# Performance work log

Measured on AMD Instinct MI355X. Metric: run time of the kernel, lower is better.

## Reference

```python
import jax, jax.numpy as jnp
import numpy as np

DIM = 512
HEADS = 8
DHEAD = 64
WIN = 128
QK_SCALE = 8.0
LN_EPS = 1e-5


def setup_inputs() -> dict:
    key = jax.random.key(0)
    ks = jax.random.split(key, 5)
    B, N = 8, 4096
    x = jax.random.normal(ks[0], (B, N, DIM), jnp.float32)
    w_qkv = jax.random.normal(ks[1], (3 * HEADS * DHEAD, DIM), jnp.float32) * 0.02
    w_out = jax.random.normal(ks[2], (DIM, HEADS * DHEAD), jnp.float32) * 0.02
    b_out = jnp.zeros((DIM,), jnp.float32)
    w_ff1 = jax.random.normal(ks[3], (4 * DIM, DIM), jnp.float32) * 0.02
    w_ff2 = jax.random.normal(ks[4], (DIM, 4 * DIM), jnp.float32) * 0.02
    return {
        'x': x, 'w_qkv': w_qkv,
        'q_scale': jnp.ones((DHEAD,), jnp.float32),
        'k_scale': jnp.ones((DHEAD,), jnp.float32),
        'w_out': w_out, 'b_out': b_out,
        'ln1_g': jnp.ones((DIM,), jnp.float32), 'ln1_b': jnp.zeros((DIM,), jnp.float32),
        'ff_ln_g': jnp.ones((DIM,), jnp.float32), 'ff_ln_b': jnp.zeros((DIM,), jnp.float32),
        'w_ff1': w_ff1, 'w_ff2': w_ff2,
    }


def _ln(x, g, b):
    m = jnp.mean(x, axis=-1, keepdims=True)
    v = jnp.mean((x - m) ** 2, axis=-1, keepdims=True)
    return (x - m) * jax.lax.rsqrt(v + LN_EPS) * g + b


def _l2norm(t):
    return t / jnp.clip(jnp.linalg.norm(t, axis=-1, keepdims=True), 1e-12)


def _rotary(t, pos):
    # t: (B, H, N, DHEAD); standard (non-xpos) rotary, half-split style
    inv_freq = 1.0 / (10000.0 ** (jnp.arange(0, DHEAD, 2, dtype=jnp.float32) / DHEAD))
    freqs = pos[:, None] * inv_freq                      # (N, DHEAD/2)
    emb = jnp.concatenate([freqs, freqs], axis=-1)       # (N, DHEAD)
    cos, sin = jnp.cos(emb), jnp.sin(emb)
    t1, t2 = t[..., : DHEAD // 2], t[..., DHEAD // 2:]
    rot = jnp.concatenate([-t2, t1], axis=-1)
    return t * cos + rot * sin


def reference(x, w_qkv, q_scale, k_scale, w_out, b_out, ln1_g, ln1_b,
              ff_ln_g, ff_ln_b, w_ff1, w_ff2):
    B, N, D = x.shape
    nw = N // WIN

    # ---- LocalMHA (prenorm, qk-rmsnorm, sliding window, causal) ----
    h = _ln(x, ln1_g, ln1_b)
    qkv = h @ w_qkv.T                                    # (B, N, 3*H*DHEAD)
    q, k, v = jnp.split(qkv, 3, axis=-1)

    def to_heads(t):
        return t.reshape(B, N, HEADS, DHEAD).transpose(0, 2, 1, 3)  # (B,H,N,d)

    q, k, v = to_heads(q), to_heads(k), to_heads(v)
    q = _l2norm(q) * q_scale
    k = _l2norm(k) * k_scale
    pos = jnp.arange(N, dtype=jnp.float32)
    q = _rotary(q, pos)
    k = _rotary(k, pos)

    # bucket into windows; keys/values look back one window
    bq = q.reshape(B, HEADS, nw, WIN, DHEAD)
    bk = k.reshape(B, HEADS, nw, WIN, DHEAD)
    bv = v.reshape(B, HEADS, nw, WIN, DHEAD)

    def look_back(t):
        prev = jnp.concatenate([jnp.zeros_like(t[:, :, :1]), t[:, :, :-1]], axis=2)
        return jnp.concatenate([prev, t], axis=3)

    kk, vv = look_back(bk), look_back(bv)

    qpos = jnp.arange(N, dtype=jnp.int32).reshape(nw, WIN)
    kprev = jnp.concatenate([jnp.full((1, WIN), -1, jnp.int32), qpos[:-1]], axis=0)
    kpos = jnp.concatenate([kprev, qpos], axis=1)
    mask = (qpos[:, :, None] >= kpos[:, None, :]) & (kpos[:, None, :] >= 0)

    sim = jnp.einsum('bhnid,bhnjd->bhnij', bq, kk) * QK_SCALE
    sim = jnp.where(mask, sim, -1e9)
    attn = jax.nn.softmax(sim, axis=-1)
    out = jnp.einsum('bhnij,bhnjd->bhnid', attn, vv)
    out = out.reshape(B, HEADS, N, DHEAD).transpose(0, 2, 1, 3).reshape(B, N, HEADS * DHEAD)
    x = x + out @ w_out.T + b_out

    # ---- FeedForward: LN -> Linear(4D, no bias) -> GELU -> Linear(D, no bias) ----
    hf = _ln(x, ff_ln_g, ff_ln_b)
    ff = jax.nn.gelu(hf @ w_ff1.T, approximate=False) @ w_ff2.T
    return x + ff
```

## Files before the change

### kernel.cpp

```cpp
#include <hip/hip_runtime.h>
#include <cstdint>
#include <cstddef>

typedef __bf16 bf16;
typedef __bf16 bf16x8 __attribute__((ext_vector_type(8)));
typedef float f32x4 __attribute__((ext_vector_type(4)));

#define DEV static __device__ __forceinline__

constexpr int BATCH = 8;
constexpr int SEQ = 4096;
constexpr int DIM = 512;
constexpr int HEADS = 8;
constexpr int DH = 64;
constexpr int WIN = 128;
constexpr int NW = SEQ / WIN;
constexpr int TOK = BATCH * SEQ;
constexpr float EPS = 1e-5f;

constexpr size_t R_EL   = (size_t)TOK * DIM;
constexpr size_t C_QKV  = 0;
constexpr size_t C_WOUT = 786432;
constexpr size_t C_WF1  = 1048576;
constexpr size_t C_WF2  = 2097152;
constexpr size_t C_SM   = 3145728;
constexpr size_t P_EL   = 3148416;

DEV void gload_lds16(const void* g, void* l) {
  __builtin_amdgcn_global_load_lds((__attribute__((address_space(1))) void*)g,
                                   (__attribute__((address_space(3))) void*)l,
                                   16, 0, 0);
}

DEV f32x4 mfma16(bf16x8 a, bf16x8 b, f32x4 c) {
  return __builtin_amdgcn_mfma_f32_16x16x32_bf16(a, b, c, 0, 0, 0);
}

DEV float fast_gelu(float v) {
  const float z = fabsf(v) * 0.7071067811865476f;
  const float t = __builtin_amdgcn_rcpf(1.0f + 0.3275911f * z);
  const float p = t * (0.254829592f +
                  t * (-0.284496736f +
                  t * (1.421413741f +
                  t * (-1.453152027f +
                  t * 1.061405429f))));
  const float e = __expf(-z * z);
  const float erfa = 1.0f - p * e;
  const float cdf = 0.5f + copysignf(0.5f * erfa, v);
  return v * cdf;
}

struct SrcPtrs { const void* p[12]; };

DEV void copy8(const void* src, long si, bf16* dst, bool f32) {
  if (f32) {
    const float4* s = (const float4*)((const float*)src + si);
    float4 a = s[0], b = s[1];
    bf16x8 o;
    o[0] = (bf16)a.x; o[1] = (bf16)a.y; o[2] = (bf16)a.z; o[3] = (bf16)a.w;
    o[4] = (bf16)b.x; o[5] = (bf16)b.y; o[6] = (bf16)b.z; o[7] = (bf16)b.w;
    *(bf16x8*)dst = o;
  } else {
    *(bf16x8*)dst = *(const bf16x8*)((const bf16*)src + si);
  }
}

__global__ __launch_bounds__(256) void ingest_kernel(SrcPtrs sp, bf16* cano) {
  const bool f32 = (((const unsigned short*)sp.p[2])[0] == 0);
  const long e = (long)threadIdx.x * 8;
  int b = blockIdx.x;
  if (b < 384)  { long o = (long)b * 2048 + e; copy8(sp.p[1], o, cano + C_QKV + o, f32); return; }
  b -= 384;
  if (b < 128)  { long o = (long)b * 2048 + e; copy8(sp.p[4], o, cano + C_WOUT + o, f32); return; }
  b -= 128;
  if (b < 512)  { long o = (long)b * 2048 + e; copy8(sp.p[10], o, cano + C_WF1 + o, f32); return; }
  b -= 512;
  if (b < 512)  { long o = (long)b * 2048 + e; copy8(sp.p[11], o, cano + C_WF2 + o, f32); return; }
  b -= 512;
  const long o = (long)b * 2048 + e;
  if (o >= 2688) return;
  const void* src; long si;
  if      (o < 64)   { src = sp.p[2]; si = o; }
  else if (o < 128)  { src = sp.p[3]; si = o - 64; }
  else if (o < 640)  { src = sp.p[5]; si = o - 128; }
  else if (o < 1152) { src = sp.p[6]; si = o - 640; }
  else if (o < 1664) { src = sp.p[7]; si = o - 1152; }
  else if (o < 2176) { src = sp.p[8]; si = o - 1664; }
  else               { src = sp.p[9]; si = o - 2176; }
  copy8(src, si, cano + C_SM + o, f32);
}

__global__ __launch_bounds__(256) void ln_kernel(const void* __restrict__ in,
                                                 const bf16* __restrict__ gg,
                                                 const bf16* __restrict__ bb,
                                                 bf16* __restrict__ out,
                                                 const unsigned short* __restrict__ probe,
                                                 int raw) {
  const int wave = threadIdx.x >> 6, lane = threadIdx.x & 63;
  const int row = blockIdx.x * 4 + wave;
  const size_t base = (size_t)row * DIM + lane * 8;
  float f[8];
  if (raw && probe[0] == 0) {
    const float4* p = (const float4*)((const float*)in + base);
    float4 a = p[0], bq = p[1];
    f[0] = a.x; f[1] = a.y; f[2] = a.z; f[3] = a.w;
    f[4] = bq.x; f[5] = bq.y; f[6] = bq.z; f[7] = bq.w;
  } else {
    bf16x8 v = *(const bf16x8*)((const bf16*)in + base);
#pragma unroll
    for (int i = 0; i < 8; ++i) f[i] = (float)v[i];
  }
  float s = 0.f, sq = 0.f;
#pragma unroll
  for (int i = 0; i < 8; ++i) { s += f[i]; sq += f[i] * f[i]; }
#pragma unroll
  for (int m = 32; m; m >>= 1) { s += __shfl_xor(s, m); sq += __shfl_xor(sq, m); }
  const float mean = s * (1.0f / DIM);
  const float var = fmaxf(sq * (1.0f / DIM) - mean * mean, 0.0f);
  const float rs = rsqrtf(var + EPS);
  bf16x8 gv = *(const bf16x8*)(gg + lane * 8);
  bf16x8 bv = *(const bf16x8*)(bb + lane * 8);
  bf16x8 o;
#pragma unroll
  for (int i = 0; i < 8; ++i) o[i] = (bf16)((f[i] - mean) * rs * (float)gv[i] + (float)bv[i]);
  *(bf16x8*)((bf16*)out + base) = o;
}

template <int MODE>
__global__ __launch_bounds__(256) void gemm_bt(const bf16* __restrict__ A,
                                               const bf16* __restrict__ Bw,
                                               bf16* __restrict__ O0, bf16* __restrict__ O1,
                                               bf16* __restrict__ O2,
                                               float* __restrict__ Of,
                                               const void* __restrict__ Xraw,
                                               const bf16* __restrict__ Xb,
                                               const bf16* __restrict__ bias,
                                               const unsigned short* __restrict__ probe,
                                               int K, int bstride, int ostride, int gx) {
  __shared__ __align__(16) bf16 smem[3 * 8192];
  const int tid = threadIdx.x;
  const int wave = tid >> 6, lane = tid & 63;
  const int l15 = lane & 15, quad = lane >> 4;
  const int id = blockIdx.x;
  const int per = gx * 8;
  const int tM = ((id / per) * 8 + (id & 7)) * 128;
  const int tN = ((id % per) >> 3) * 128;
  const int wM = (wave >> 1) * 64, wN = (wave & 1) * 64;
  f32x4 acc[4][4];
  const f32x4 z = {0.f, 0.f, 0.f, 0.f};
#pragma unroll
  for (int i = 0; i < 4; ++i)
#pragma unroll
    for (int j = 0; j < 4; ++j) acc[i][j] = z;

  auto stage = [&](int t, int p) {
    const int k0 = t * 32;
    bf16* dA = smem + p * 8192;
    bf16* dB = dA + 4096;
#pragma unroll
    for (int tt = 0; tt < 2; ++tt) {
      const int c = tid + tt * 256;
      const int row = c >> 2, cc = (c & 3) * 8;
      gload_lds16(A + (size_t)(tM + row) * K + k0 + cc, &dA[c * 8]);
      gload_lds16(Bw + (size_t)(tN + row) * bstride + k0 + cc, &dB[c * 8]);
    }
  };

  const int nt = K >> 5;
  stage(0, 0);
  stage(1, 1);
  __builtin_amdgcn_sched_barrier(0);
  asm volatile("s_waitcnt vmcnt(4)" ::: "memory");
  __builtin_amdgcn_s_barrier();
  __builtin_amdgcn_sched_barrier(0);

  int cur = 0;
  for (int t = 0; t < nt; ++t) {
    if (t + 2 < nt) {
      int nx = cur + 2; if (nx >= 3) nx -= 3;
      stage(t + 2, nx);
    }
    const bf16* As = smem + cur * 8192;
    const bf16* Bs = As + 4096;
    bf16x8 aF[4], bF[4];
#pragma unroll
    for (int i = 0; i < 4; ++i) aF[i] = *(const bf16x8*)&As[(wM + i * 16 + l15) * 32 + quad * 8];
#pragma unroll
    for (int j = 0; j < 4; ++j) bF[j] = *(const bf16x8*)&Bs[(wN + j * 16 + l15) * 32 + quad * 8];
#pragma unroll
    for (int i = 0; i < 4; ++i)
#pragma unroll
      for (int j = 0; j < 4; ++j) acc[i][j] = mfma16(aF[i], bF[j], acc[i][j]);
    if (t < nt - 1) {
      __builtin_amdgcn_sched_barrier(0);
      if (t + 2 < nt) asm volatile("s_waitcnt vmcnt(4)" ::: "memory");
      else            asm volatile("s_waitcnt vmcnt(0)" ::: "memory");
      __builtin_amdgcn_s_barrier();
      __builtin_amdgcn_sched_barrier(0);
    }
    ++cur; if (cur == 3) cur = 0;
  }
  bf16* eb = smem + cur * 8192;

  if constexpr (MODE == 0) {
    bf16* ob = eb + wave * 1152;
    const int colbase = tN + wN;
    const int which = colbase >> 9;
    const int head = (colbase >> 6) & 7;
    bf16* dst = which == 0 ? O0 : (which == 1 ? O1 : O2);
    const int ch = lane & 7;
    float scv[8], invf[8];
    if (which < 2) {
      const bf16* sc = which ? bias : Xb;
      bf16x8 s8 = *(const bf16x8*)(sc + ch * 8);
#pragma unroll
      for (int u = 0; u < 8; ++u) {
        scv[u] = (float)s8[u] * (which == 0 ? 8.0f : 1.0f);
        invf[u] = exp2f(-(float)((ch & 3) * 8 + u) * (13.287712379549449f / 32.0f));
      }
    }
#pragma unroll
    for (int i = 0; i < 4; ++i) {
#pragma unroll
      for (int j = 0; j < 4; ++j)
#pragma unroll
        for (int r = 0; r < 4; ++r)
          ob[(quad * 4 + r) * 72 + j * 16 + l15] = (bf16)acc[i][j][r];
#pragma unroll
      for (int t = 0; t < 2; ++t) {
        const int rr = t * 8 + (lane >> 3);
        const int rowg = tM + wM + i * 16 + rr;
        bf16x8 ov = *(const bf16x8*)&ob[rr * 72 + ch * 8];
        float f[8];
#pragma unroll
        for (int u = 0; u < 8; ++u) f[u] = (float)ov[u];
        if (which < 2) {
          float ss = 0.f;
#pragma unroll
          for (int u = 0; u < 8; ++u) ss += f[u] * f[u];
          ss += __shfl_xor(ss, 1); ss += __shfl_xor(ss, 2); ss += __shfl_xor(ss, 4);
          const float rs = 1.0f / fmaxf(sqrtf(ss), 1e-12f);
#pragma unroll
          for (int u = 0; u < 8; ++u) f[u] *= rs * scv[u];
          float pf[8];
#pragma unroll
          for (int u = 0; u < 8; ++u) pf[u] = __shfl_xor(f[u], 4);
          const float pos = (float)(rowg & (SEQ - 1));
#pragma unroll
          for (int u = 0; u < 8; ++u) {
            float sn, cs;
            __sincosf(pos * invf[u], &sn, &cs);
            const float rot = (ch < 4) ? -pf[u] : pf[u];
            f[u] = f[u] * cs + rot * sn;
          }
        }
        bf16x8 o8;
#pragma unroll
        for (int u = 0; u < 8; ++u) o8[u] = (bf16)f[u];
        const int bb = rowg >> 12, n = rowg & (SEQ - 1);
        *(bf16x8*)(dst + ((size_t)(bb * HEADS + head) * SEQ + n) * DH + ch * 8) = o8;
      }
    }
    return;
  }

  if constexpr (MODE == 1 || MODE == 2) {
    bf16* ob = eb + wave * 1152;
    const int ch = lane & 7;
    bf16x8 bias8;
    bool xf32 = false;
    if constexpr (MODE == 1) {
      bias8 = *(const bf16x8*)(bias + tN + wN + ch * 8);
      xf32 = (probe[0] == 0);
    }
#pragma unroll
    for (int i = 0; i < 4; ++i) {
#pragma unroll
      for (int j = 0; j < 4; ++j)
#pragma unroll
        for (int r = 0; r < 4; ++r)
          ob[(quad * 4 + r) * 72 + j * 16 + l15] = (bf16)acc[i][j][r];
#pragma unroll
      for (int t = 0; t < 2; ++t) {
        const int rr = t * 8 + (lane >> 3);
        const int rowg = tM + wM + i * 16 + rr;
        bf16x8 ov = *(const bf16x8*)&ob[rr * 72 + ch * 8];
        bf16x8 o8;
        if constexpr (MODE == 1) {
          const size_t idx = (size_t)rowg * DIM + tN + wN + ch * 8;
          float xr[8];
          if (xf32) {
            const float4* xp = (const float4*)((const float*)Xraw + idx);
            float4 a = xp[0], bq = xp[1];
            xr[0] = a.x; xr[1] = a.y; xr[2] = a.z; xr[3] = a.w;
            xr[4] = bq.x; xr[5] = bq.y; xr[6] = bq.z; xr[7] = bq.w;
          } else {
            bf16x8 xv = *(const bf16x8*)((const bf16*)Xraw + idx);
#pragma unroll
            for (int u = 0; u < 8; ++u) xr[u] = (float)xv[u];
          }
#pragma unroll
          for (int u = 0; u < 8; ++u) o8[u] = (bf16)((float)ov[u] + xr[u] + (float)bias8[u]);
          *(bf16x8*)(O0 + idx) = o8;
        } else {
#pragma unroll
          for (int u = 0; u < 8; ++u) o8[u] = (bf16)fast_gelu((float)ov[u]);
          *(bf16x8*)(O0 + (size_t)rowg * ostride + tN + wN + ch * 8) = o8;
        }
      }
    }
    return;
  }

  if constexpr (MODE == 3 || MODE == 4) {
    float* obf = (float*)eb + wave * 1024;
    const int ch = lane & 7;
#pragma unroll
    for (int i = 0; i < 4; ++i) {
#pragma unroll
      for (int j = 0; j < 4; ++j)
#pragma unroll
        for (int r = 0; r < 4; ++r)
          obf[(quad * 4 + r) * 64 + j * 16 + l15] = acc[i][j][r];
#pragma unroll
      for (int t = 0; t < 2; ++t) {
        const int rr = t * 8 + (lane >> 3);
        const int rowg = tM + wM + i * 16 + rr;
        const size_t idx = (size_t)rowg * DIM + tN + wN + ch * 8;
        const float4* rp = (const float4*)&obf[rr * 64 + ch * 8];
        float4 a = rp[0], b = rp[1];
        float f[8] = {a.x, a.y, a.z, a.w, b.x, b.y, b.z, b.w};
        if constexpr (MODE == 3) {
          bf16x8 xv = *(const bf16x8*)(Xb + idx);
#pragma unroll
          for (int u = 0; u < 8; ++u) f[u] += (float)xv[u];
        } else {
          const float4* op = (const float4*)(Of + idx);
          float4 oa = op[0], ob4 = op[1];
          f[0] += oa.x; f[1] += oa.y; f[2] += oa.z; f[3] += oa.w;
          f[4] += ob4.x; f[5] += ob4.y; f[6] += ob4.z; f[7] += ob4.w;
        }
        float4 o0 = {f[0], f[1], f[2], f[3]}, o1 = {f[4], f[5], f[6], f[7]};
        ((float4*)(Of + idx))[0] = o0;
        ((float4*)(Of + idx))[1] = o1;
      }
    }
    return;
  }
}

__global__ __launch_bounds__(256, 3) void attn_kernel(const bf16* __restrict__ q,
                                                      const bf16* __restrict__ k,
                                                      const bf16* __restrict__ v,
                                                      bf16* __restrict__ ao) {
  __shared__ __align__(16) bf16 kv[256 * 72];
  __shared__ __align__(16) bf16 pbuf[4][16 * 136];
  const int w = blockIdx.x, h = blockIdx.y, b = blockIdx.z;
  const int tid = threadIdx.x;
  const int wv = tid >> 6, lane = tid & 63;
  const int l15 = lane & 15, quad = lane >> 4;
  const size_t bh = (size_t)b * HEADS + h;
  const bf16* qb = q + bh * SEQ * DH;
  const bf16* kb = k + bh * SEQ * DH;
  const bf16* vb = v + bh * SEQ * DH;
  const int t0 = (w - 1) * WIN;

#pragma unroll
  for (int it = 0; it < 8; ++it) {
    const int c = it * 256 + tid;
    const int tok = c >> 3, ch = c & 7;
    int gt = t0 + tok; gt = gt < 0 ? 0 : gt;
    *(bf16x8*)&kv[tok * 72 + ch * 8] = *(const bf16x8*)(kb + (size_t)gt * DH + ch * 8);
  }
  bf16x8 aQ[2][2];
#pragma unroll
  for (int qt = 0; qt < 2; ++qt) {
    const int qtok = w * WIN + wv * 32 + qt * 16 + l15;
#pragma unroll
    for (int ks = 0; ks < 2; ++ks)
      aQ[qt][ks] = *(const bf16x8*)(qb + (size_t)qtok * DH + ks * 32 + quad * 8);
  }
  int gtv = t0 + tid; gtv = gtv < 0 ? 0 : gtv;
  bf16x8 vld[8];
#pragma unroll
  for (int dg = 0; dg < 8; ++dg)
    vld[dg] = *(const bf16x8*)(vb + (size_t)gtv * DH + dg * 8);
  __syncthreads();

  bf16x8 aP[2][8];
#pragma unroll
  for (int qt = 0; qt < 2; ++qt) {
    f32x4 sreg[16];
#pragma unroll
    for (int nt = 0; nt < 16; ++nt) {
      f32x4 a = {0.f, 0.f, 0.f, 0.f};
#pragma unroll
      for (int ks = 0; ks < 2; ++ks) {
        bf16x8 bK = *(const bf16x8*)&kv[(nt * 16 + l15) * 72 + ks * 32 + quad * 8];
        a = mfma16(aQ[qt][ks], bK, a);
      }
      sreg[nt] = a;
    }
    const int qlb = wv * 32 + qt * 16 + quad * 4;
    float rinv[4];
#pragma unroll
    for (int r = 0; r < 4; ++r) {
      const int ql = qlb + r;
      float sum = 0.f;
#pragma unroll
      for (int nt = 0; nt < 16; ++nt) {
        const int j = nt * 16 + l15;
        const bool valid = (nt < 8) ? (w > 0) : (ql >= j - WIN);
        const float p = valid ? __expf(sreg[nt][r]) : 0.0f;
        sreg[nt][r] = p;
        sum += p;
      }
#pragma unroll
      for (int m = 8; m; m >>= 1) sum += __shfl_xor(sum, m);
      rinv[r] = 1.0f / sum;
    }
#pragma unroll
    for (int half = 0; half < 2; ++half) {
#pragma unroll
      for (int ntw = 0; ntw < 8; ++ntw)
#pragma unroll
        for (int r = 0; r < 4; ++r)
          pbuf[wv][(quad * 4 + r) * 136 + ntw * 16 + l15] =
              (bf16)(sreg[half * 8 + ntw][r] * rinv[r]);
#pragma unroll
      for (int kk = 0; kk < 4; ++kk)
        aP[qt][half * 4 + kk] = *(const bf16x8*)&pbuf[wv][l15 * 136 + kk * 32 + quad * 8];
    }
  }
  __syncthreads();

#pragma unroll
  for (int dg = 0; dg < 8; ++dg)
#pragma unroll
    for (int i = 0; i < 8; ++i)
      kv[(dg * 8 + i) * 264 + tid] = vld[dg][i];
  __syncthreads();

#pragma unroll
  for (int qt = 0; qt < 2; ++qt) {
#pragma unroll
    for (int dt = 0; dt < 4; ++dt) {
      f32x4 o = {0.f, 0.f, 0.f, 0.f};
#pragma unroll
      for (int ks2 = 0; ks2 < 8; ++ks2) {
        bf16x8 bV = *(const bf16x8*)&kv[(dt * 16 + l15) * 264 + ks2 * 32 + quad * 8];
        o = mfma16(aP[qt][ks2], bV, o);
      }
#pragma unroll
      for (int r = 0; r < 4; ++r)
        pbuf[wv][(quad * 4 + r) * 136 + dt * 16 + l15] = (bf16)o[r];
    }
#pragma unroll
    for (int t = 0; t < 2; ++t) {
      const int rr = t * 8 + (lane >> 3), ch = lane & 7;
      bf16x8 ov = *(const bf16x8*)&pbuf[wv][rr * 136 + ch * 8];
      const int tok = w * WIN + wv * 32 + qt * 16 + rr;
      *(bf16x8*)(ao + ((size_t)b * SEQ + tok) * DIM + h * DH + ch * 8) = ov;
    }
  }
}

extern "C" void kernel_launch(void* const* d_in, const int* in_sizes, int n_in,
                              void* d_out, int out_size, void* d_ws, size_t ws_size,
                              hipStream_t stream) {
  (void)in_sizes; (void)n_in; (void)out_size;
  float* out = (float*)d_out;
  bf16* cano = (bf16*)d_ws;
  const unsigned short* probe = (const unsigned short*)d_in[2];

  SrcPtrs sp;
  for (int i = 0; i < 12; ++i) sp.p[i] = d_in[i];

  bf16* slot0 = cano + P_EL;
  bf16* slot1 = cano + P_EL + R_EL;
  bf16* slot2 = cano + P_EL + 2 * R_EL;
  bf16* slot3 = cano + P_EL + 3 * R_EL;

  const bf16* qsc  = cano + C_SM + 0;
  const bf16* ksc  = cano + C_SM + 64;
  const bf16* bout = cano + C_SM + 128;
  const bf16* l1g  = cano + C_SM + 640;
  const bf16* l1b  = cano + C_SM + 1152;
  const bf16* lfg  = cano + C_SM + 1664;
  const bf16* lfb  = cano + C_SM + 2176;

  ingest_kernel<<<1538, 256, 0, stream>>>(sp, cano);
  ln_kernel<<<TOK / 4, 256, 0, stream>>>(d_in[0], l1g, l1b, slot0, probe, 1);
  gemm_bt<0><<<12 * 256, 256, 0, stream>>>(slot0, cano + C_QKV, slot1, slot2, slot3,
                                           nullptr, nullptr, qsc, ksc, probe,
                                           DIM, DIM, 0, 12);
  attn_kernel<<<dim3(NW, HEADS, BATCH), 256, 0, stream>>>(slot1, slot2, slot3, slot0);
  gemm_bt<1><<<4 * 256, 256, 0, stream>>>(slot0, cano + C_WOUT, slot1, nullptr, nullptr,
                                          nullptr, d_in[0], nullptr, bout, probe,
                                          DIM, DIM, 0, 4);
  ln_kernel<<<TOK / 4, 256, 0, stream>>>(slot1, lfg, lfb, slot0, probe, 0);

  const bool big = ws_size >= (size_t)(P_EL + 6 * R_EL) * 2;
  if (big) {
    bf16* f1 = slot2;
    gemm_bt<2><<<16 * 256, 256, 0, stream>>>(slot0, cano + C_WF1, f1, nullptr, nullptr,
                                             nullptr, nullptr, nullptr, nullptr, probe,
                                             DIM, DIM, 2048, 16);
    gemm_bt<3><<<4 * 256, 256, 0, stream>>>(f1, cano + C_WF2, nullptr, nullptr, nullptr,
                                            out, nullptr, slot1, nullptr, probe,
                                            2048, 2048, 0, 4);
  } else {
    bf16* f1h = slot2;
    for (int half = 0; half < 2; ++half) {
      const bf16* w1h = cano + C_WF1 + (size_t)half * 1024 * DIM;
      const bf16* w2h = cano + C_WF2 + (size_t)half * 1024;
      gemm_bt<2><<<8 * 256, 256, 0, stream>>>(slot0, w1h, f1h, nullptr, nullptr,
                                              nullptr, nullptr, nullptr, nullptr, probe,
                                              DIM, DIM, 1024, 8);
      if (half == 0)
        gemm_bt<3><<<4 * 256, 256, 0, stream>>>(f1h, w2h, nullptr, nullptr, nullptr,
                                                out, nullptr, slot1, nullptr, probe,
                                                1024, 2048, 0, 4);
      else
        gemm_bt<4><<<4 * 256, 256, 0, stream>>>(f1h, w2h, nullptr, nullptr, nullptr,
                                                out, nullptr, nullptr, nullptr, probe,
                                                1024, 2048, 0, 4);
    }
  }
}
```

Baseline: 505.9 us.

## Enlarge GEMM block tile to 256x128 with eight waves and dynamic LDS

Doubles the M dimension of each GEMM block tile from 128 to 256 rows and runs 8 waves (512 threads) per block. Each block stages a 256x32 A tile and a 128x32 B tile per k-step in dynamically allocated shared memory, so each B tile is reused by twice as many rows. The vmcnt waits are adjusted to the new per-stage load count, and the fp32 epilogue now spans two pipeline buffers. The aim is to cut global/L2 traffic for B and the number of blocks, at the cost of more LDS per block and possibly lower occupancy.

```diff
diff --git a/kernel.cpp b/kernel.cpp
--- a/kernel.cpp
+++ b/kernel.cpp
@@ -127,7 +127,7 @@
 }
 
 template <int MODE>
-__global__ __launch_bounds__(256) void gemm_bt(const bf16* __restrict__ A,
+__global__ __launch_bounds__(512) void gemm_bt(const bf16* __restrict__ A,
                                                const bf16* __restrict__ Bw,
                                                bf16* __restrict__ O0, bf16* __restrict__ O1,
                                                bf16* __restrict__ O2,
@@ -137,15 +137,15 @@
                                                const bf16* __restrict__ bias,
                                                const unsigned short* __restrict__ probe,
                                                int K, int bstride, int ostride, int gx) {
-  __shared__ __align__(16) bf16 smem[3 * 8192];
+  extern __shared__ __align__(16) bf16 smem[];
   const int tid = threadIdx.x;
-  const int wave = tid >> 6, lane = tid & 63;
+  const int wid = tid >> 6, lane = tid & 63;
   const int l15 = lane & 15, quad = lane >> 4;
   const int id = blockIdx.x;
   const int per = gx * 8;
-  const int tM = ((id / per) * 8 + (id & 7)) * 128;
+  const int tM = ((id / per) * 8 + (id & 7)) * 256;
   const int tN = ((id % per) >> 3) * 128;
-  const int wM = (wave >> 1) * 64, wN = (wave & 1) * 64;
+  const int wM = (wid >> 1) * 64, wN = (wid & 1) * 64;
   f32x4 acc[4][4];
   const f32x4 z = {0.f, 0.f, 0.f, 0.f};
 #pragma unroll
@@ -155,13 +155,18 @@
 
   auto stage = [&](int t, int p) {
     const int k0 = t * 32;
-    bf16* dA = smem + p * 8192;
-    bf16* dB = dA + 4096;
-#pragma unroll
-    for (int tt = 0; tt < 2; ++tt) {
-      const int c = tid + tt * 256;
-      const int row = c >> 2, cc = (c & 3) * 8;
+    bf16* dA = smem + p * 12288;
+    bf16* dB = dA + 8192;
+    {
+      const int c = tid, row = c >> 2, cc = (c & 3) * 8;
       gload_lds16(A + (size_t)(tM + row) * K + k0 + cc, &dA[c * 8]);
+    }
+    {
+      const int c = tid + 512, row = c >> 2, cc = (c & 3) * 8;
+      gload_lds16(A + (size_t)(tM + row) * K + k0 + cc, &dA[c * 8]);
+    }
+    {
+      const int c = tid, row = c >> 2, cc = (c & 3) * 8;
       gload_lds16(Bw + (size_t)(tN + row) * bstride + k0 + cc, &dB[c * 8]);
     }
   };
@@ -170,7 +175,7 @@
   stage(0, 0);
   stage(1, 1);
   __builtin_amdgcn_sched_barrier(0);
-  asm volatile("s_waitcnt vmcnt(4)" ::: "memory");
+  asm volatile("s_waitcnt vmcnt(3)" ::: "memory");
   __builtin_amdgcn_s_barrier();
   __builtin_amdgcn_sched_barrier(0);
 
@@ -180,8 +185,8 @@
       int nx = cur + 2; if (nx >= 3) nx -= 3;
       stage(t + 2, nx);
     }
-    const bf16* As = smem + cur * 8192;
-    const bf16* Bs = As + 4096;
+    const bf16* As = smem + cur * 12288;
+    const bf16* Bs = As + 8192;
     bf16x8 aF[4], bF[4];
 #pragma unroll
     for (int i = 0; i < 4; ++i) aF[i] = *(const bf16x8*)&As[(wM + i * 16 + l15) * 32 + quad * 8];
@@ -193,17 +198,19 @@
       for (int j = 0; j < 4; ++j) acc[i][j] = mfma16(aF[i], bF[j], acc[i][j]);
     if (t < nt - 1) {
       __builtin_amdgcn_sched_barrier(0);
-      if (t + 2 < nt) asm volatile("s_waitcnt vmcnt(4)" ::: "memory");
+      if (t + 2 < nt) asm volatile("s_waitcnt vmcnt(3)" ::: "memory");
       else            asm volatile("s_waitcnt vmcnt(0)" ::: "memory");
       __builtin_amdgcn_s_barrier();
       __builtin_amdgcn_sched_barrier(0);
     }
     ++cur; if (cur == 3) cur = 0;
   }
-  bf16* eb = smem + cur * 8192;
+  const int q0 = nt % 3;
+  int q1 = q0 + 1; if (q1 == 3) q1 = 0;
+  bf16* eb = smem + q0 * 12288;
 
   if constexpr (MODE == 0) {
-    bf16* ob = eb + wave * 1152;
+    bf16* ob = eb + wid * 1152;
     const int colbase = tN + wN;
     const int which = colbase >> 9;
     const int head = (colbase >> 6) & 7;
@@ -265,7 +272,7 @@
   }
 
   if constexpr (MODE == 1 || MODE == 2) {
-    bf16* ob = eb + wave * 1152;
+    bf16* ob = eb + wid * 1152;
     const int ch = lane & 7;
     bf16x8 bias8;
     bool xf32 = false;
@@ -313,7 +320,9 @@
   }
 
   if constexpr (MODE == 3 || MODE == 4) {
-    float* obf = (float*)eb + wave * 1024;
+    float* obf = (wid < 6)
+        ? (float*)(smem + q0 * 12288) + wid * 1024
+        : (float*)(smem + q1 * 12288) + (wid - 6) * 1024;
     const int ch = lane & 7;
 #pragma unroll
     for (int i = 0; i < 4; ++i) {
@@ -489,42 +498,53 @@
   const bf16* lfg  = cano + C_SM + 1664;
   const bf16* lfb  = cano + C_SM + 2176;
 
+  constexpr int LDSB = 3 * 12288 * 2;
+  static bool attr_done = false;
+  if (!attr_done) {
+    hipFuncSetAttribute((const void*)gemm_bt<0>, hipFuncAttributeMaxDynamicSharedMemorySize, LDSB);
+    hipFuncSetAttribute((const void*)gemm_bt<1>, hipFuncAttributeMaxDynamicSharedMemorySize, LDSB);
+    hipFuncSetAttribute((const void*)gemm_bt<2>, hipFuncAttributeMaxDynamicSharedMemorySize, LDSB);
+    hipFuncSetAttribute((const void*)gemm_bt<3>, hipFuncAttributeMaxDynamicSharedMemorySize, LDSB);
+    hipFuncSetAttribute((const void*)gemm_bt<4>, hipFuncAttributeMaxDynamicSharedMemorySize, LDSB);
+    attr_done = true;
+  }
+
   ingest_kernel<<<1538, 256, 0, stream>>>(sp, cano);
   ln_kernel<<<TOK / 4, 256, 0, stream>>>(d_in[0], l1g, l1b, slot0, probe, 1);
-  gemm_bt<0><<<12 * 256, 256, 0, stream>>>(slot0, cano + C_QKV, slot1, slot2, slot3,
-                                           nullptr, nullptr, qsc, ksc, probe,
-                                           DIM, DIM, 0, 12);
+  gemm_bt<0><<<16 * 96, 512, LDSB, stream>>>(slot0, cano + C_QKV, slot1, slot2, slot3,
+                                             nullptr, nullptr, qsc, ksc, probe,
+                                             DIM, DIM, 0, 12);
   attn_kernel<<<dim3(NW, HEADS, BATCH), 256, 0, stream>>>(slot1, slot2, slot3, slot0);
-  gemm_bt<1><<<4 * 256, 256, 0, stream>>>(slot0, cano + C_WOUT, slot1, nullptr, nullptr,
-                                          nullptr, d_in[0], nullptr, bout, probe,
-                                          DIM, DIM, 0, 4);
+  gemm_bt<1><<<16 * 32, 512, LDSB, stream>>>(slot0, cano + C_WOUT, slot1, nullptr, nullptr,
+                                             nullptr, d_in[0], nullptr, bout, probe,
+                                             DIM, DIM, 0, 4);
   ln_kernel<<<TOK / 4, 256, 0, stream>>>(slot1, lfg, lfb, slot0, probe, 0);
 
   const bool big = ws_size >= (size_t)(P_EL + 6 * R_EL) * 2;
   if (big) {
     bf16* f1 = slot2;
-    gemm_bt<2><<<16 * 256, 256, 0, stream>>>(slot0, cano + C_WF1, f1, nullptr, nullptr,
-                                             nullptr, nullptr, nullptr, nullptr, probe,
-                                             DIM, DIM, 2048, 16);
-    gemm_bt<3><<<4 * 256, 256, 0, stream>>>(f1, cano + C_WF2, nullptr, nullptr, nullptr,
-                                            out, nullptr, slot1, nullptr, probe,
-                                            2048, 2048, 0, 4);
+    gemm_bt<2><<<16 * 128, 512, LDSB, stream>>>(slot0, cano + C_WF1, f1, nullptr, nullptr,
+                                                nullptr, nullptr, nullptr, nullptr, probe,
+                                                DIM, DIM, 2048, 16);
+    gemm_bt<3><<<16 * 32, 512, LDSB, stream>>>(f1, cano + C_WF2, nullptr, nullptr, nullptr,
+                                               out, nullptr, slot1, nullptr, probe,
+                                               2048, 2048, 0, 4);
   } else {
     bf16* f1h = slot2;
     for (int half = 0; half < 2; ++half) {
       const bf16* w1h = cano + C_WF1 + (size_t)half * 1024 * DIM;
       const bf16* w2h = cano + C_WF2 + (size_t)half * 1024;
-      gemm_bt<2><<<8 * 256, 256, 0, stream>>>(slot0, w1h, f1h, nullptr, nullptr,
-                                              nullptr, nullptr, nullptr, nullptr, probe,
-                                              DIM, DIM, 1024, 8);
+      gemm_bt<2><<<16 * 64, 512, LDSB, stream>>>(slot0, w1h, f1h, nullptr, nullptr,
+                                                 nullptr, nullptr, nullptr, nullptr, probe,
+                                                 DIM, DIM, 1024, 8);
       if (half == 0)
-        gemm_bt<3><<<4 * 256, 256, 0, stream>>>(f1h, w2h, nullptr, nullptr, nullptr,
-                                                out, nullptr, slot1, nullptr, probe,
-                                                1024, 2048, 0, 4);
+        gemm_bt<3><<<16 * 32, 512, LDSB, stream>>>(f1h, w2h, nullptr, nullptr, nullptr,
+                                                   out, nullptr, slot1, nullptr, probe,
+                                                   1024, 2048, 0, 4);
       else
-        gemm_bt<4><<<4 * 256, 256, 0, stream>>>(f1h, w2h, nullptr, nullptr, nullptr,
-                                                out, nullptr, nullptr, nullptr, probe,
-                                                1024, 2048, 0, 4);
-    }
-  }
-}
+        gemm_bt<4><<<16 * 32, 512, LDSB, stream>>>(f1h, w2h, nullptr, nullptr, nullptr,
+                                                   out, nullptr, nullptr, nullptr, probe,
+                                                   1024, 2048, 0, 4);
+    }
+  }
+}
```

New measurement: 497.4 us. Within noise of the previous version (-1.7%).
